# Performance work log

Hardware: AMD Instinct MI355X
Metric: run time of the kernel (lower is better)

## Reference

```python
import jax, jax.numpy as jnp
import numpy as np
import math

B, T, D, H = 2, 2048, 1024, 16


def _layernorm(x, gamma, beta, eps=1e-5):
    mu = jnp.mean(x, axis=-1, keepdims=True)
    var = jnp.var(x, axis=-1, keepdims=True)
    return (x - mu) * jax.lax.rsqrt(var + eps) * gamma + beta


def setup_inputs() -> dict:
    key = jax.random.key(0)
    ks = jax.random.split(key, 12)
    s = 1.0 / math.sqrt(D)
    return {
        "x": jax.random.normal(ks[0], (B, T, D), dtype=jnp.float32),
        "src_mask": jax.random.randint(ks[1], (B, T, T), 0, 2, dtype=jnp.int32),
        "ln_gamma": jnp.ones((D,), jnp.float32),
        "ln_beta": jnp.zeros((D,), jnp.float32),
        "Wq": jax.random.normal(ks[2], (D, D), jnp.float32) * s,
        "bq": jnp.zeros((D,), jnp.float32),
        "Wk": jax.random.normal(ks[3], (D, D), jnp.float32) * s,
        "bk": jnp.zeros((D,), jnp.float32),
        "Wv": jax.random.normal(ks[4], (D, D), jnp.float32) * s,
        "bv": jnp.zeros((D,), jnp.float32),
        "Wo": jax.random.normal(ks[5], (D, D), jnp.float32) * s,
        "bo": jnp.zeros((D,), jnp.float32),
    }


def reference(x, src_mask, ln_gamma, ln_beta, Wq, bq, Wk, bk, Wv, bv, Wo, bo):
    Bx, Tx, Dx = x.shape
    dh = Dx // H
    xn = _layernorm(x, ln_gamma, ln_beta)  # single LN; the three calls are identical
    q = (xn @ Wq + bq).reshape(Bx, Tx, H, dh)
    k = (xn @ Wk + bk).reshape(Bx, Tx, H, dh)
    v = (xn @ Wv + bv).reshape(Bx, Tx, H, dh)
    # scores: B, n, m, h
    attn = jnp.einsum('bnhd,bmhd->bnmh', q, k) / math.sqrt(dh)
    attn = attn + (1.0 - src_mask.astype(attn.dtype))[..., None] * -100000.0
    weight = jax.nn.softmax(attn, axis=2)
    y = jnp.einsum('bnmh,bmhd->bnhd', weight, v).reshape(Bx, Tx, Dx)
    return x + (y @ Wo + bo)
```

## Files before the change

### kernel.cpp

```cpp
#include <hip/hip_runtime.h>
#include <hip/hip_bf16.h>
#include <stdint.h>

#define Tq 2048
#define Dd 1024
#define Hh 16

typedef unsigned short u16;
typedef __attribute__((ext_vector_type(8))) short short8;
typedef __attribute__((ext_vector_type(4))) float f32x4;

__device__ __forceinline__ u16 f2bf(float f) {
  union { float f; unsigned u; } v; v.f = f;
  unsigned r = (v.u + 0x7fffu + ((v.u >> 16) & 1u)) >> 16;
  return (u16)r;
}

__device__ __forceinline__ unsigned pk2bf(float a, float b) {
  __hip_bfloat162 h = __float22bfloat162_rn(float2{a, b});
  union { __hip_bfloat162 h; unsigned u; } c; c.h = h;
  return c.u;
}

__device__ __forceinline__ void load_lds16(const void* g, void* l) {
  __builtin_amdgcn_global_load_lds(
      (const __attribute__((address_space(1))) unsigned*)g,
      (__attribute__((address_space(3))) unsigned*)l, 16, 0, 0);
}

__device__ __forceinline__ f32x4 mfma16(short8 a, short8 b, f32x4 c) {
  return __builtin_amdgcn_mfma_f32_16x16x32_bf16(a, b, c, 0, 0, 0);
}

__device__ __forceinline__ void permswap(unsigned& xx, unsigned& yy) {
#if __has_builtin(__builtin_amdgcn_permlane32_swap) && \
    __has_builtin(__builtin_amdgcn_permlane16_swap)
  typedef __attribute__((ext_vector_type(2))) unsigned uint2v;
  uint2v t0 = __builtin_amdgcn_permlane32_swap(xx, yy, false, false);
  uint2v t1 = __builtin_amdgcn_permlane16_swap(t0[0], t0[1], false, false);
  xx = t1[0];
  yy = t1[1];
#else
  asm volatile(
      "s_nop 1\n\t"
      "v_permlane32_swap_b32 %0, %1\n\t"
      "s_nop 1\n\t"
      "v_permlane16_swap_b32 %0, %1\n\t"
      "s_nop 1"
      : "+v"(xx), "+v"(yy));
#endif
}

__global__ __launch_bounds__(256) void prep_kernel(
    const float* __restrict__ x, const float* __restrict__ gamma,
    const float* __restrict__ beta, u16* __restrict__ xn,
    const float* __restrict__ W0, const float* __restrict__ W1,
    const float* __restrict__ W2, const float* __restrict__ W3,
    u16* __restrict__ o_qkv, u16* __restrict__ o_o,
    const int* __restrict__ mask, uint32_t* __restrict__ bits,
    const float* __restrict__ bq, const float* __restrict__ bk,
    const float* __restrict__ bv, float* __restrict__ bias3) {
  __shared__ float t[32][33];
  int idx = blockIdx.x;
  int tid = threadIdx.x;
  if (idx < 4096) {
    int row = idx;
    const float4 v = ((const float4*)(x + (size_t)row * Dd))[tid];
    float s = v.x + v.y + v.z + v.w;
    float s2 = v.x * v.x + v.y * v.y + v.z * v.z + v.w * v.w;
#pragma unroll
    for (int off = 1; off < 64; off <<= 1) {
      s += __shfl_xor(s, off);
      s2 += __shfl_xor(s2, off);
    }
    int w = tid >> 6;
    if ((tid & 63) == 0) { t[0][w] = s; t[0][4 + w] = s2; }
    __syncthreads();
    s = t[0][0] + t[0][1] + t[0][2] + t[0][3];
    s2 = t[0][4] + t[0][5] + t[0][6] + t[0][7];
    float mu = s * (1.0f / Dd);
    float var = s2 * (1.0f / Dd) - mu * mu;
    float rstd = rsqrtf(var + 1e-5f);
    const float4 g = ((const float4*)gamma)[tid];
    const float4 bb = ((const float4*)beta)[tid];
    union { unsigned us[2]; uint2 u2; } o;
    o.us[0] = pk2bf((v.x - mu) * rstd * g.x + bb.x, (v.y - mu) * rstd * g.y + bb.y);
    o.us[1] = pk2bf((v.z - mu) * rstd * g.z + bb.z, (v.w - mu) * rstd * g.w + bb.w);
    *(uint2*)(xn + (size_t)row * Dd + tid * 4) = o.u2;
  } else if (idx < 8192) {
    int ti = idx - 4096;
    int z = ti >> 10, i = ti & 1023;
    const float* W = (z == 0) ? W0 : (z == 1) ? W1 : (z == 2) ? W2 : W3;
    u16* out = (z < 3) ? (o_qkv + (size_t)z * 1024 * 1024) : o_o;
    int k0 = (i & 31) * 32, n0 = (i >> 5) * 32;
    int tx = tid & 31, ty = tid >> 5;
#pragma unroll
    for (int j = 0; j < 4; ++j)
      t[ty + j * 8][tx] = W[(size_t)(k0 + ty + j * 8) * Dd + n0 + tx];
    __syncthreads();
#pragma unroll
    for (int j = 0; j < 4; ++j)
      out[(size_t)(n0 + ty + j * 8) * Dd + k0 + tx] = f2bf(t[tx][ty + j * 8]);
  } else if (idx < 9216) {
    int m = idx - 8192;
    int b = m >> 9, rest = m & 511;
    int qw = rest >> 3, kblk = rest & 7;
    int k = kblk * 256 + tid;
    const int* mp = mask + ((size_t)b * Tq + qw * 32) * Tq + k;
    uint32_t wv = 0;
#pragma unroll
    for (int j = 0; j < 32; ++j) wv |= (mp[(size_t)j * Tq] ? 1u : 0u) << j;
    bits[((size_t)b * 64 + qw) * Tq + k] = wv;
  } else {
    int i = (idx - 9216) * 256 + tid;
    float v = (i < 1024) ? bq[i] : (i < 2048) ? bk[i - 1024] : bv[i - 2048];
    bias3[i] = v;
  }
}

__global__ __launch_bounds__(256) void vt_kernel(
    const u16* __restrict__ qkv, u16* __restrict__ vt) {
  __shared__ u16 t[32][33];
  int bh = blockIdx.z;
  int b = bh >> 4, h = bh & 15;
  int t0 = blockIdx.x * 32, d0 = blockIdx.y * 32;
  int tx = threadIdx.x & 31, ty = threadIdx.x >> 5;
#pragma unroll
  for (int i = 0; i < 4; ++i)
    t[ty + i * 8][tx] =
        qkv[(size_t)(b * Tq + t0 + ty + i * 8) * 3072 + 2048 + h * 64 + d0 + tx];
  __syncthreads();
#pragma unroll
  for (int i = 0; i < 4; ++i)
    vt[((size_t)bh * 64 + d0 + ty + i * 8) * Tq + t0 + tx] = t[tx][ty + i * 8];
}

template <int MODE, int MT>
__global__ __launch_bounds__(256) void gemm_bt(
    const u16* __restrict__ A, const u16* __restrict__ Bt,
    const float* __restrict__ bias, const float* __restrict__ resid,
    void* __restrict__ Cout, int ldc, int K) {
  constexpr int MTI = MT / 32;
  constexpr int ACALLS = MT / 64;
  __shared__ u16 As[MT * 32];
  __shared__ u16 Bs[128 * 32];
  int tid = threadIdx.x;
  int lane = tid & 63, w = tid >> 6;
  int l16 = lane & 15, quad = lane >> 4;
  int wm = w >> 1, wn = w & 1;
  int m0 = blockIdx.y * MT, n0 = blockIdx.x * 128;
  int srow = lane >> 2, scol = (lane & 3) << 3;
  const u16* ga0 = A + (size_t)(m0 + srow) * K + scol;
  const u16* gb0 = Bt + (size_t)(n0 + srow) * K + scol;
  f32x4 acc[MTI][4];
#pragma unroll
  for (int i = 0; i < MTI; ++i)
#pragma unroll
    for (int j = 0; j < 4; ++j) acc[i][j] = {0.f, 0.f, 0.f, 0.f};

  for (int k0 = 0; k0 < K; k0 += 32) {
    __syncthreads();
#pragma unroll
    for (int c = 0; c < ACALLS; ++c) {
      int rb = w * (MT / 4) + c * 16;
      load_lds16(ga0 + (size_t)rb * K + k0, (char*)As + rb * 64);
    }
#pragma unroll
    for (int c = 0; c < 2; ++c) {
      int rb = w * 32 + c * 16;
      load_lds16(gb0 + (size_t)rb * K + k0, (char*)Bs + rb * 64);
    }
    __syncthreads();
    short8 af[MTI], bf[4];
#pragma unroll
    for (int mt = 0; mt < MTI; ++mt)
      af[mt] = *(const short8*)&As[(wm * (MT / 2) + mt * 16 + l16) * 32 + quad * 8];
#pragma unroll
    for (int nt = 0; nt < 4; ++nt)
      bf[nt] = *(const short8*)&Bs[(wn * 64 + nt * 16 + l16) * 32 + quad * 8];
#pragma unroll
    for (int mt = 0; mt < MTI; ++mt)
#pragma unroll
      for (int nt = 0; nt < 4; ++nt)
        acc[mt][nt] = mfma16(af[mt], bf[nt], acc[mt][nt]);
  }
#pragma unroll
  for (int nt = 0; nt < 4; ++nt) {
    int col = n0 + wn * 64 + nt * 16 + l16;
    float bv = bias[col];
    float scl = (MODE == 0 && col < 1024) ? 0.18033688011112042f : 1.0f;
#pragma unroll
    for (int mt = 0; mt < MTI; ++mt) {
#pragma unroll
      for (int r = 0; r < 4; ++r) {
        int row = m0 + wm * (MT / 2) + mt * 16 + quad * 4 + r;
        size_t idx = (size_t)row * ldc + col;
        float vv = (acc[mt][nt][r] + bv) * scl;
        if (MODE == 0)
          ((u16*)Cout)[idx] = f2bf(vv);
        else
          ((float*)Cout)[idx] = vv + resid[idx];
      }
    }
  }
}

__global__ __launch_bounds__(256, 4) void attn_kernel(
    const u16* __restrict__ qkv, const u16* __restrict__ vt,
    const uint32_t* __restrict__ mbits, u16* __restrict__ ybuf) {
  __shared__ u16 Ks[2][64 * 64];
  __shared__ u16 Vs[2][64 * 64];
  int tid = threadIdx.x;
  int lane = tid & 63, w = tid >> 6;
  int l16 = lane & 15, quad = lane >> 4;
  int x7 = l16 & 7;
  int qt = blockIdx.x, h = blockIdx.y, b = blockIdx.z;
  int qbase = qt * 64 + w * 16;
  const u16* Qb = qkv + (size_t)b * Tq * 3072 + h * 64;
  const u16* Kb = Qb + 1024;
  const u16* Vb = vt + ((size_t)(b * Hh + h)) * 64 * Tq;
  const uint32_t* Mrow = mbits + ((size_t)b * 64 + (qbase >> 5)) * Tq;
  int shift = (qbase & 31) + l16;
  int shl = 31 - shift;

  int half = (w & 1) * 32;
  int r8 = lane >> 3;
  int phys = lane & 7;
  int chunk = phys ^ r8;
  bool isK = (w < 2);

  short8 qf[2];
#pragma unroll
  for (int ks = 0; ks < 2; ++ks)
    qf[ks] = *(const short8*)&Qb[(size_t)(qbase + l16) * 3072 + ks * 32 + quad * 8];

  f32x4 acc[4];
#pragma unroll
  for (int j = 0; j < 4; ++j) acc[j] = {0.f, 0.f, 0.f, 0.f};
  float lsa[4] = {0.f, 0.f, 0.f, 0.f};

  auto stage = [&](int buf, int k0) {
    if (isK) {
#pragma unroll
      for (int j = 0; j < 4; ++j)
        load_lds16(Kb + (size_t)(k0 + half + j * 8 + r8) * 3072 + chunk * 8,
                   (char*)&Ks[buf][0] + (half + j * 8) * 128);
    } else {
#pragma unroll
      for (int j = 0; j < 4; ++j)
        load_lds16(Vb + (size_t)(half + j * 8 + r8) * Tq + k0 + chunk * 8,
                   (char*)&Vs[buf][0] + (half + j * 8) * 128);
    }
  };

  stage(0, 0);

  for (int kt = 0; kt < 32; ++kt) {
    int k0 = kt * 64;
    int buf = kt & 1;
    __syncthreads();
    uint32_t mv[4][4];
#pragma unroll
    for (int mt = 0; mt < 4; ++mt) {
      uint4 m4 = *(const uint4*)&Mrow[k0 + mt * 16 + quad * 4];
      mv[mt][0] = m4.x; mv[mt][1] = m4.y; mv[mt][2] = m4.z; mv[mt][3] = m4.w;
    }
    if (kt < 31) stage(buf ^ 1, k0 + 64);
    const u16* Kt = Ks[buf];
    const u16* Vtile = Vs[buf];
    f32x4 s[4];
#pragma unroll
    for (int i = 0; i < 4; ++i) s[i] = {0.f, 0.f, 0.f, 0.f};
#pragma unroll
    for (int mt = 0; mt < 4; ++mt)
#pragma unroll
      for (int ks = 0; ks < 2; ++ks) {
        short8 kf = *(const short8*)&Kt[(mt * 16 + l16) * 64 +
                                        (((ks << 2) | quad) ^ x7) * 8];
        s[mt] = mfma16(kf, qf[ks], s[mt]);
      }
    unsigned c[4][2];
#pragma unroll
    for (int mt = 0; mt < 4; ++mt) {
      float p[4];
#pragma unroll
      for (int r = 0; r < 4; ++r) {
        float e = __builtin_amdgcn_exp2f(s[mt][r]);
        int keep = (int)(mv[mt][r] << shl) >> 31;
        union { float f; int i; } u; u.f = e; u.i &= keep;
        p[r] = u.f;
        lsa[r] += u.f;
      }
      c[mt][0] = pk2bf(p[0], p[1]);
      c[mt][1] = pk2bf(p[2], p[3]);
    }
    short8 pf[2];
#pragma unroll
    for (int ks = 0; ks < 2; ++ks) {
      union { unsigned u[4]; short8 s8; } P;
#pragma unroll
      for (int hh = 0; hh < 2; ++hh) {
        unsigned xx = c[2 * ks][hh], yy = c[2 * ks + 1][hh];
        permswap(xx, yy);
        P.u[hh] = xx;
        P.u[2 + hh] = yy;
      }
      pf[ks] = P.s8;
    }
#pragma unroll
    for (int ks = 0; ks < 2; ++ks)
#pragma unroll
      for (int nt2 = 0; nt2 < 4; ++nt2) {
        short8 vf = *(const short8*)&Vtile[(nt2 * 16 + l16) * 64 +
                                           (((ks << 2) | quad) ^ x7) * 8];
        acc[nt2] = mfma16(pf[ks], vf, acc[nt2]);
      }
  }
  float lst = (lsa[0] + lsa[1]) + (lsa[2] + lsa[3]);
  lst += __shfl_xor(lst, 16);
  lst += __shfl_xor(lst, 32);
#pragma unroll
  for (int r = 0; r < 4; ++r) {
    float li = 1.0f / __shfl(lst, quad * 4 + r);
    size_t row = (size_t)b * Tq + qbase + quad * 4 + r;
#pragma unroll
    for (int nt2 = 0; nt2 < 4; ++nt2)
      ybuf[row * Dd + h * 64 + nt2 * 16 + l16] = f2bf(acc[nt2][r] * li);
  }
}

extern "C" void kernel_launch(void* const* d_in, const int* in_sizes, int n_in,
                              void* d_out, int out_size, void* d_ws, size_t ws_size,
                              hipStream_t stream) {
  (void)in_sizes; (void)n_in; (void)out_size; (void)ws_size;
  const float* x = (const float*)d_in[0];
  const int* mask = (const int*)d_in[1];
  const float* gamma = (const float*)d_in[2];
  const float* beta = (const float*)d_in[3];
  const float* Wq = (const float*)d_in[4];
  const float* bq = (const float*)d_in[5];
  const float* Wk = (const float*)d_in[6];
  const float* bk = (const float*)d_in[7];
  const float* Wv = (const float*)d_in[8];
  const float* bv = (const float*)d_in[9];
  const float* Wo = (const float*)d_in[10];
  const float* bo = (const float*)d_in[11];
  float* out = (float*)d_out;
  char* ws = (char*)d_ws;

  constexpr size_t SZ_XN = (size_t)4096 * 1024 * 2;
  constexpr size_t SZ_WTQ = (size_t)3072 * 1024 * 2;
  constexpr size_t SZ_WOT = (size_t)1024 * 1024 * 2;
  constexpr size_t SZ_B3 = 3072 * 4;
  constexpr size_t SZ_QKV = (size_t)4096 * 3072 * 2;
  constexpr size_t SZ_MBITS = (size_t)2 * 64 * 2048 * 4;
  constexpr size_t SZ_VT = (size_t)2 * 16 * 64 * 2048 * 2;
  size_t off = 0;
  u16* xn = (u16*)(ws + off); off += SZ_XN;
  u16* wtqkv = (u16*)(ws + off); off += SZ_WTQ;
  u16* wot = (u16*)(ws + off); off += SZ_WOT;
  float* bias3 = (float*)(ws + off); off += SZ_B3;
  u16* qkvb = (u16*)(ws + off); off += SZ_QKV;
  uint32_t* mbits = (uint32_t*)(ws + off); off += SZ_MBITS;
  u16* vtb = (u16*)(ws + off); off += SZ_VT;
  u16* ybuf = (u16*)(ws + off);

  prep_kernel<<<dim3(9228), dim3(256), 0, stream>>>(
      x, gamma, beta, xn, Wq, Wk, Wv, Wo, wtqkv, wot, mask, mbits, bq, bk, bv,
      bias3);
  gemm_bt<0, 128><<<dim3(24, 32), dim3(256), 0, stream>>>(
      xn, wtqkv, bias3, nullptr, qkvb, 3072, 1024);
  vt_kernel<<<dim3(64, 2, 32), dim3(256), 0, stream>>>(qkvb, vtb);
  attn_kernel<<<dim3(32, 16, 2), dim3(256), 0, stream>>>(qkvb, vtb, mbits, ybuf);
  gemm_bt<1, 64><<<dim3(8, 64), dim3(256), 0, stream>>>(
      ybuf, wot, bo, x, out, 1024, 1024);
}
```

Before: 250.1 us.

## Split key tiles across warps in attention and reduce partials via LDS

After: 260.2 us. +4.1%, slower.

```diff
diff --git a/kernel.cpp b/kernel.cpp
--- a/kernel.cpp
+++ b/kernel.cpp
@@ -205,7 +205,7 @@
   }
 }
 
-__global__ __launch_bounds__(256, 4) void attn_kernel(
+__global__ __launch_bounds__(256, 5) void attn_kernel(
     const u16* __restrict__ qkv, const u16* __restrict__ vt,
     const uint32_t* __restrict__ mbits, u16* __restrict__ ybuf) {
   __shared__ u16 Ks[2][64 * 64];
@@ -215,12 +215,14 @@
   int l16 = lane & 15, quad = lane >> 4;
   int x7 = l16 & 7;
   int qt = blockIdx.x, h = blockIdx.y, b = blockIdx.z;
-  int qbase = qt * 64 + w * 16;
+  int qw = w & 1;
+  int kw = w >> 1;
+  int qbase = qt * 32;
   const u16* Qb = qkv + (size_t)b * Tq * 3072 + h * 64;
   const u16* Kb = Qb + 1024;
   const u16* Vb = vt + ((size_t)(b * Hh + h)) * 64 * Tq;
   const uint32_t* Mrow = mbits + ((size_t)b * 64 + (qbase >> 5)) * Tq;
-  int shift = (qbase & 31) + l16;
+  int shift = qw * 16 + l16;
   int shl = 31 - shift;
 
   int half = (w & 1) * 32;
@@ -232,7 +234,8 @@
   short8 qf[2];
 #pragma unroll
   for (int ks = 0; ks < 2; ++ks)
-    qf[ks] = *(const short8*)&Qb[(size_t)(qbase + l16) * 3072 + ks * 32 + quad * 8];
+    qf[ks] = *(const short8*)&Qb[(size_t)(qbase + qw * 16 + l16) * 3072 +
+                                 ks * 32 + quad * 8];
 
   f32x4 acc[4];
 #pragma unroll
@@ -259,73 +262,90 @@
     int k0 = kt * 64;
     int buf = kt & 1;
     __syncthreads();
-    uint32_t mv[4][4];
-#pragma unroll
-    for (int mt = 0; mt < 4; ++mt) {
-      uint4 m4 = *(const uint4*)&Mrow[k0 + mt * 16 + quad * 4];
-      mv[mt][0] = m4.x; mv[mt][1] = m4.y; mv[mt][2] = m4.z; mv[mt][3] = m4.w;
+    uint32_t mv[2][4];
+#pragma unroll
+    for (int mtl = 0; mtl < 2; ++mtl) {
+      uint4 m4 = *(const uint4*)&Mrow[k0 + (2 * kw + mtl) * 16 + quad * 4];
+      mv[mtl][0] = m4.x; mv[mtl][1] = m4.y; mv[mtl][2] = m4.z; mv[mtl][3] = m4.w;
     }
     if (kt < 31) stage(buf ^ 1, k0 + 64);
     const u16* Kt = Ks[buf];
     const u16* Vtile = Vs[buf];
-    f32x4 s[4];
-#pragma unroll
-    for (int i = 0; i < 4; ++i) s[i] = {0.f, 0.f, 0.f, 0.f};
-#pragma unroll
-    for (int mt = 0; mt < 4; ++mt)
+    f32x4 s[2];
+#pragma unroll
+    for (int i = 0; i < 2; ++i) s[i] = {0.f, 0.f, 0.f, 0.f};
+#pragma unroll
+    for (int mtl = 0; mtl < 2; ++mtl) {
+      int mt = 2 * kw + mtl;
 #pragma unroll
       for (int ks = 0; ks < 2; ++ks) {
         short8 kf = *(const short8*)&Kt[(mt * 16 + l16) * 64 +
                                         (((ks << 2) | quad) ^ x7) * 8];
-        s[mt] = mfma16(kf, qf[ks], s[mt]);
+        s[mtl] = mfma16(kf, qf[ks], s[mtl]);
       }
-    unsigned c[4][2];
-#pragma unroll
-    for (int mt = 0; mt < 4; ++mt) {
+    }
+    unsigned c[2][2];
+#pragma unroll
+    for (int mtl = 0; mtl < 2; ++mtl) {
       float p[4];
 #pragma unroll
       for (int r = 0; r < 4; ++r) {
-        float e = __builtin_amdgcn_exp2f(s[mt][r]);
-        int keep = (int)(mv[mt][r] << shl) >> 31;
+        float e = __builtin_amdgcn_exp2f(s[mtl][r]);
+        int keep = (int)(mv[mtl][r] << shl) >> 31;
         union { float f; int i; } u; u.f = e; u.i &= keep;
         p[r] = u.f;
         lsa[r] += u.f;
       }
-      c[mt][0] = pk2bf(p[0], p[1]);
-      c[mt][1] = pk2bf(p[2], p[3]);
-    }
-    short8 pf[2];
-#pragma unroll
-    for (int ks = 0; ks < 2; ++ks) {
+      c[mtl][0] = pk2bf(p[0], p[1]);
+      c[mtl][1] = pk2bf(p[2], p[3]);
+    }
+    short8 pf;
+    {
       union { unsigned u[4]; short8 s8; } P;
 #pragma unroll
       for (int hh = 0; hh < 2; ++hh) {
-        unsigned xx = c[2 * ks][hh], yy = c[2 * ks + 1][hh];
+        unsigned xx = c[0][hh], yy = c[1][hh];
         permswap(xx, yy);
         P.u[hh] = xx;
         P.u[2 + hh] = yy;
       }
-      pf[ks] = P.s8;
-    }
-#pragma unroll
-    for (int ks = 0; ks < 2; ++ks)
-#pragma unroll
-      for (int nt2 = 0; nt2 < 4; ++nt2) {
-        short8 vf = *(const short8*)&Vtile[(nt2 * 16 + l16) * 64 +
-                                           (((ks << 2) | quad) ^ x7) * 8];
-        acc[nt2] = mfma16(pf[ks], vf, acc[nt2]);
-      }
+      pf = P.s8;
+    }
+#pragma unroll
+    for (int nt2 = 0; nt2 < 4; ++nt2) {
+      short8 vf = *(const short8*)&Vtile[(nt2 * 16 + l16) * 64 +
+                                         (((kw << 2) | quad) ^ x7) * 8];
+      acc[nt2] = mfma16(pf, vf, acc[nt2]);
+    }
   }
   float lst = (lsa[0] + lsa[1]) + (lsa[2] + lsa[3]);
-  lst += __shfl_xor(lst, 16);
-  lst += __shfl_xor(lst, 32);
-#pragma unroll
-  for (int r = 0; r < 4; ++r) {
-    float li = 1.0f / __shfl(lst, quad * 4 + r);
-    size_t row = (size_t)b * Tq + qbase + quad * 4 + r;
+  float* cb = (float*)&Ks[0][0];
+  int cbase = (qw * 64 + lane) * 20;
+  __syncthreads();
+  if (kw == 1) {
 #pragma unroll
     for (int nt2 = 0; nt2 < 4; ++nt2)
-      ybuf[row * Dd + h * 64 + nt2 * 16 + l16] = f2bf(acc[nt2][r] * li);
+#pragma unroll
+      for (int r = 0; r < 4; ++r) cb[cbase + nt2 * 4 + r] = acc[nt2][r];
+    cb[cbase + 16] = lst;
+  }
+  __syncthreads();
+  if (kw == 0) {
+#pragma unroll
+    for (int nt2 = 0; nt2 < 4; ++nt2)
+#pragma unroll
+      for (int r = 0; r < 4; ++r) acc[nt2][r] += cb[cbase + nt2 * 4 + r];
+    lst += cb[cbase + 16];
+    lst += __shfl_xor(lst, 16);
+    lst += __shfl_xor(lst, 32);
+#pragma unroll
+    for (int r = 0; r < 4; ++r) {
+      float li = 1.0f / __shfl(lst, quad * 4 + r);
+      size_t row = (size_t)b * Tq + qbase + qw * 16 + quad * 4 + r;
+#pragma unroll
+      for (int nt2 = 0; nt2 < 4; ++nt2)
+        ybuf[row * Dd + h * 64 + nt2 * 16 + l16] = f2bf(acc[nt2][r] * li);
+    }
   }
 }
 
@@ -371,7 +391,7 @@
   gemm_bt<0, 128><<<dim3(24, 32), dim3(256), 0, stream>>>(
       xn, wtqkv, bias3, nullptr, qkvb, 3072, 1024);
   vt_kernel<<<dim3(64, 2, 32), dim3(256), 0, stream>>>(qkvb, vtb);
-  attn_kernel<<<dim3(32, 16, 2), dim3(256), 0, stream>>>(qkvb, vtb, mbits, ybuf);
+  attn_kernel<<<dim3(64, 16, 2), dim3(256), 0, stream>>>(qkvb, vtb, mbits, ybuf);
   gemm_bt<1, 64><<<dim3(8, 64), dim3(256), 0, stream>>>(
       ybuf, wot, bo, x, out, 1024, 1024);
 }
```

## Compute V transposed directly via swapped GEMM and row-sum via MFMA

Applied to the files above, without the earlier changes.

Measured after the change: 257.5 us. 3.0% more time.

```diff
diff --git a/kernel.cpp b/kernel.cpp
--- a/kernel.cpp
+++ b/kernel.cpp
@@ -118,23 +118,6 @@
   }
 }
 
-__global__ __launch_bounds__(256) void vt_kernel(
-    const u16* __restrict__ qkv, u16* __restrict__ vt) {
-  __shared__ u16 t[32][33];
-  int bh = blockIdx.z;
-  int b = bh >> 4, h = bh & 15;
-  int t0 = blockIdx.x * 32, d0 = blockIdx.y * 32;
-  int tx = threadIdx.x & 31, ty = threadIdx.x >> 5;
-#pragma unroll
-  for (int i = 0; i < 4; ++i)
-    t[ty + i * 8][tx] =
-        qkv[(size_t)(b * Tq + t0 + ty + i * 8) * 3072 + 2048 + h * 64 + d0 + tx];
-  __syncthreads();
-#pragma unroll
-  for (int i = 0; i < 4; ++i)
-    vt[((size_t)bh * 64 + d0 + ty + i * 8) * Tq + t0 + tx] = t[tx][ty + i * 8];
-}
-
 template <int MODE, int MT>
 __global__ __launch_bounds__(256) void gemm_bt(
     const u16* __restrict__ A, const u16* __restrict__ Bt,
@@ -187,7 +170,7 @@
 #pragma unroll
   for (int nt = 0; nt < 4; ++nt) {
     int col = n0 + wn * 64 + nt * 16 + l16;
-    float bv = bias[col];
+    float bcol = (MODE == 2) ? 0.f : bias[col];
     float scl = (MODE == 0 && col < 1024) ? 0.18033688011112042f : 1.0f;
 #pragma unroll
     for (int mt = 0; mt < MTI; ++mt) {
@@ -195,11 +178,12 @@
       for (int r = 0; r < 4; ++r) {
         int row = m0 + wm * (MT / 2) + mt * 16 + quad * 4 + r;
         size_t idx = (size_t)row * ldc + col;
+        float bv = (MODE == 2) ? bias[row] : bcol;
         float vv = (acc[mt][nt][r] + bv) * scl;
-        if (MODE == 0)
+        if (MODE == 1)
+          ((float*)Cout)[idx] = vv + resid[idx];
+        else
           ((u16*)Cout)[idx] = f2bf(vv);
-        else
-          ((float*)Cout)[idx] = vv + resid[idx];
       }
     }
   }
@@ -216,12 +200,11 @@
   int x7 = l16 & 7;
   int qt = blockIdx.x, h = blockIdx.y, b = blockIdx.z;
   int qbase = qt * 64 + w * 16;
-  const u16* Qb = qkv + (size_t)b * Tq * 3072 + h * 64;
+  const u16* Qb = qkv + (size_t)b * Tq * 2048 + h * 64;
   const u16* Kb = Qb + 1024;
-  const u16* Vb = vt + ((size_t)(b * Hh + h)) * 64 * Tq;
+  const u16* Vb = vt + (size_t)(h * 64) * 4096 + b * 2048;
   const uint32_t* Mrow = mbits + ((size_t)b * 64 + (qbase >> 5)) * Tq;
   int shift = (qbase & 31) + l16;
-  int shl = 31 - shift;
 
   int half = (w & 1) * 32;
   int r8 = lane >> 3;
@@ -232,23 +215,26 @@
   short8 qf[2];
 #pragma unroll
   for (int ks = 0; ks < 2; ++ks)
-    qf[ks] = *(const short8*)&Qb[(size_t)(qbase + l16) * 3072 + ks * 32 + quad * 8];
+    qf[ks] = *(const short8*)&Qb[(size_t)(qbase + l16) * 2048 + ks * 32 + quad * 8];
+
+  const short8 vones = {0x3F80, 0x3F80, 0x3F80, 0x3F80,
+                        0x3F80, 0x3F80, 0x3F80, 0x3F80};
 
   f32x4 acc[4];
 #pragma unroll
   for (int j = 0; j < 4; ++j) acc[j] = {0.f, 0.f, 0.f, 0.f};
-  float lsa[4] = {0.f, 0.f, 0.f, 0.f};
+  f32x4 acc_s = {0.f, 0.f, 0.f, 0.f};
 
   auto stage = [&](int buf, int k0) {
     if (isK) {
 #pragma unroll
       for (int j = 0; j < 4; ++j)
-        load_lds16(Kb + (size_t)(k0 + half + j * 8 + r8) * 3072 + chunk * 8,
+        load_lds16(Kb + (size_t)(k0 + half + j * 8 + r8) * 2048 + chunk * 8,
                    (char*)&Ks[buf][0] + (half + j * 8) * 128);
     } else {
 #pragma unroll
       for (int j = 0; j < 4; ++j)
-        load_lds16(Vb + (size_t)(half + j * 8 + r8) * Tq + k0 + chunk * 8,
+        load_lds16(Vb + (size_t)(half + j * 8 + r8) * 4096 + k0 + chunk * 8,
                    (char*)&Vs[buf][0] + (half + j * 8) * 128);
     }
   };
@@ -286,10 +272,9 @@
 #pragma unroll
       for (int r = 0; r < 4; ++r) {
         float e = __builtin_amdgcn_exp2f(s[mt][r]);
-        int keep = (int)(mv[mt][r] << shl) >> 31;
+        int keep = __builtin_amdgcn_sbfe((int)mv[mt][r], (unsigned)shift, 1u);
         union { float f; int i; } u; u.f = e; u.i &= keep;
         p[r] = u.f;
-        lsa[r] += u.f;
       }
       c[mt][0] = pk2bf(p[0], p[1]);
       c[mt][1] = pk2bf(p[2], p[3]);
@@ -307,6 +292,8 @@
       }
       pf[ks] = P.s8;
     }
+    acc_s = mfma16(pf[0], vones, acc_s);
+    acc_s = mfma16(pf[1], vones, acc_s);
 #pragma unroll
     for (int ks = 0; ks < 2; ++ks)
 #pragma unroll
@@ -316,12 +303,9 @@
         acc[nt2] = mfma16(pf[ks], vf, acc[nt2]);
       }
   }
-  float lst = (lsa[0] + lsa[1]) + (lsa[2] + lsa[3]);
-  lst += __shfl_xor(lst, 16);
-  lst += __shfl_xor(lst, 32);
 #pragma unroll
   for (int r = 0; r < 4; ++r) {
-    float li = 1.0f / __shfl(lst, quad * 4 + r);
+    float li = 1.0f / acc_s[r];
     size_t row = (size_t)b * Tq + qbase + quad * 4 + r;
 #pragma unroll
     for (int nt2 = 0; nt2 < 4; ++nt2)
@@ -352,9 +336,9 @@
   constexpr size_t SZ_WTQ = (size_t)3072 * 1024 * 2;
   constexpr size_t SZ_WOT = (size_t)1024 * 1024 * 2;
   constexpr size_t SZ_B3 = 3072 * 4;
-  constexpr size_t SZ_QKV = (size_t)4096 * 3072 * 2;
+  constexpr size_t SZ_QKV = (size_t)4096 * 2048 * 2;
   constexpr size_t SZ_MBITS = (size_t)2 * 64 * 2048 * 4;
-  constexpr size_t SZ_VT = (size_t)2 * 16 * 64 * 2048 * 2;
+  constexpr size_t SZ_VT = (size_t)1024 * 4096 * 2;
   size_t off = 0;
   u16* xn = (u16*)(ws + off); off += SZ_XN;
   u16* wtqkv = (u16*)(ws + off); off += SZ_WTQ;
@@ -368,9 +352,11 @@
   prep_kernel<<<dim3(9228), dim3(256), 0, stream>>>(
       x, gamma, beta, xn, Wq, Wk, Wv, Wo, wtqkv, wot, mask, mbits, bq, bk, bv,
       bias3);
-  gemm_bt<0, 128><<<dim3(24, 32), dim3(256), 0, stream>>>(
-      xn, wtqkv, bias3, nullptr, qkvb, 3072, 1024);
-  vt_kernel<<<dim3(64, 2, 32), dim3(256), 0, stream>>>(qkvb, vtb);
+  gemm_bt<0, 128><<<dim3(16, 32), dim3(256), 0, stream>>>(
+      xn, wtqkv, bias3, nullptr, qkvb, 2048, 1024);
+  gemm_bt<2, 128><<<dim3(32, 8), dim3(256), 0, stream>>>(
+      wtqkv + (size_t)2 * 1024 * 1024, xn, bias3 + 2048, nullptr, vtb, 4096,
+      1024);
   attn_kernel<<<dim3(32, 16, 2), dim3(256), 0, stream>>>(qkvb, vtb, mbits, ybuf);
   gemm_bt<1, 64><<<dim3(8, 64), dim3(256), 0, stream>>>(
       ybuf, wot, bo, x, out, 1024, 1024);
```
